# Performance work log

Measured on AMD Instinct MI355X. Metric: run time of the kernel, lower is better.

## Reference

```python
import jax, jax.numpy as jnp
import numpy as np

NW = 11       # num_windows per side
HEADS = 4
TOPK = 4
KVP = 4       # kv_per_window (adaptive maxpool output side)
BN_EPS = 1e-5
CLAMP = 0.12


def silu(x):
    return x * jax.nn.sigmoid(x)


def conv2d(x, w, b=None, groups=1, pad=0):
    y = jax.lax.conv_general_dilated(
        x, w, (1, 1), [(pad, pad), (pad, pad)],
        dimension_numbers=('NCHW', 'OIHW', 'NCHW'), feature_group_count=groups)
    if b is not None:
        y = y + b[None, :, None, None]
    return y


def grid_sample_bilinear(img, grid):
    # img (N,C,H,W), grid (N,Hg,Wg,2) in (x,y) order, align_corners=True.
    N, C, H, W = img.shape
    gx = (grid[..., 0] + 1.0) * 0.5 * (W - 1)
    gy = (grid[..., 1] + 1.0) * 0.5 * (H - 1)
    x0f = jnp.floor(gx)
    y0f = jnp.floor(gy)
    wx = (gx - x0f)[:, None]   # (N,1,Hg,Wg)
    wy = (gy - y0f)[:, None]
    x0 = jnp.clip(x0f.astype(jnp.int32), 0, W - 1)
    x1 = jnp.clip(x0 + 1, 0, W - 1)
    y0 = jnp.clip(y0f.astype(jnp.int32), 0, H - 1)
    y1 = jnp.clip(y0 + 1, 0, H - 1)
    gather = jax.vmap(lambda im, yi, xi: im[:, yi, xi])  # (C,Hg,Wg) per batch
    v00 = gather(img, y0, x0)
    v01 = gather(img, y0, x1)
    v10 = gather(img, y1, x0)
    v11 = gather(img, y1, x1)
    return (v00 * (1 - wx) * (1 - wy) + v01 * wx * (1 - wy)
            + v10 * (1 - wx) * wy + v11 * wx * wy)


def reference(x, q_w, q_b, kv_w, kv_b, off_dw_w, off_dw_b, off_bn_g, off_bn_b,
              off_pw_w, sec_w, sec_b):
    N, C, Hin, Win = x.shape
    pad_b = (-Hin) % NW
    pad_r = (-Win) % NW
    xp = jnp.pad(x, ((0, 0), (0, 0), (0, pad_b), (0, pad_r)))
    H, W = xp.shape[2], xp.shape[3]
    hw, ww = H // NW, W // NW
    p2, w2 = NW * NW, hw * ww
    qk_dim = C
    dh = C // HEADS
    scale = qk_dim ** (-0.5)

    # query projection (Conv+folded-BN+SiLU)
    q = silu(conv2d(xp, q_w, q_b))                       # (N,C,H,W)

    # deformable offset predictor: dwconv k9 -> BN(eval) -> 1x1 -> 2 channels
    t = conv2d(q, off_dw_w, off_dw_b, groups=C, pad=off_dw_w.shape[-1] // 2)
    t = (t / jnp.sqrt(1.0 + BN_EPS)) * off_bn_g[None, :, None, None] \
        + off_bn_b[None, :, None, None]
    offset = conv2d(t, off_pw_w)                         # (N,2,H,W)
    offset = jnp.transpose(offset, (0, 2, 3, 1))         # (N,H,W,2) as (y,x)

    # normalized reference points (torch linspace(0.5, s-0.5, s)/(s-1)*2-1)
    ry = jnp.linspace(0.5, H - 0.5, H) / (H - 1.0) * 2.0 - 1.0
    rx = jnp.linspace(0.5, W - 0.5, W) / (W - 1.0) * 2.0 - 1.0
    ref = jnp.stack(jnp.meshgrid(ry, rx, indexing='ij'), -1)  # (H,W,2) y,x
    pos = jnp.clip(offset + ref[None], -CLAMP, CLAMP)
    x_samp = grid_sample_bilinear(xp, pos[..., ::-1])    # grid in (x,y)

    kv = silu(conv2d(x_samp, kv_w, kv_b))                # (N,2C,H,W)

    def windowize(t):  # (N,Cc,H,W) -> (N,p2,hw,ww,Cc), p2 = j*NW+i
        Cc = t.shape[1]
        t = t.reshape(N, Cc, NW, hw, NW, ww)
        return jnp.transpose(t, (0, 2, 4, 3, 5, 1)).reshape(N, p2, hw, ww, Cc)

    q_win = windowize(q)                                 # (N,p2,hw,ww,C)
    kv_win = windowize(kv)                               # (N,p2,hw,ww,2C)

    # adaptive max-pool (hw,ww)->(KVP,KVP): evenly divisible here
    kvd = kv_win.reshape(N, p2, KVP, hw // KVP, KVP, ww // KVP, 2 * C)
    kvd = kvd.max(axis=(3, 5)).reshape(N, p2, KVP * KVP, 2 * C)

    # window-level top-k routing on detached window means
    qwin = jax.lax.stop_gradient(q_win.mean((2, 3)))                 # (N,p2,C)
    kwin = jax.lax.stop_gradient(kv_win[..., :qk_dim].mean((2, 3)))  # (N,p2,C)
    logit = jnp.einsum('npc,nqc->npq', qwin * scale, kwin)
    top_val, top_idx = jax.lax.top_k(logit, TOPK)        # (N,p2,TOPK)
    r_weight = jax.nn.softmax(top_val, -1)               # computed but unused (hard routing)

    # KV gather of routed windows
    kv_sel = kvd[jnp.arange(N)[:, None, None], top_idx]  # (N,p2,TOPK,16,2C)
    kw2 = TOPK * KVP * KVP
    k_sel = kv_sel[..., :qk_dim].reshape(N, p2, kw2, HEADS, dh)
    v_sel = kv_sel[..., qk_dim:].reshape(N, p2, kw2, HEADS, dh)
    q_pix = q_win.reshape(N, p2, w2, HEADS, dh)

    attn = jnp.einsum('npwhd,npkhd->nphwk', q_pix * scale, k_sel)
    attn = jax.nn.softmax(attn, -1)
    out = jnp.einsum('nphwk,npkhd->npwhd', attn, v_sel).reshape(N, p2, w2, C)

    # side conv enhancement on V, in full spatial layout
    v_full = kv_win[..., qk_dim:].reshape(N, NW, NW, hw, ww, C)
    v_full = jnp.transpose(v_full, (0, 5, 1, 3, 2, 4)).reshape(N, C, H, W)
    sec = conv2d(v_full, sec_w, sec_b, groups=C, pad=sec_w.shape[-1] // 2)
    sec = jnp.transpose(sec, (0, 2, 3, 1))               # (N,H,W,C)

    out = out.reshape(N, NW, NW, hw, ww, C)
    out = jnp.transpose(out, (0, 1, 3, 2, 4, 5)).reshape(N, H, W, C)
    out = (out + sec)[:, :Hin, :Win]
    return jnp.transpose(out, (0, 3, 1, 2))


def setup_inputs() -> dict:
    key = jax.random.key(0)
    ks = jax.random.split(key, 8)
    C = 128
    x = jax.random.normal(ks[0], (2, C, 352, 352), jnp.float32)
    q_w = jax.random.normal(ks[1], (C, C, 1, 1), jnp.float32) * 0.02
    q_b = jnp.zeros((C,), jnp.float32)
    kv_w = jax.random.normal(ks[2], (2 * C, C, 1, 1), jnp.float32) * 0.02
    kv_b = jnp.zeros((2 * C,), jnp.float32)
    off_dw_w = jax.random.normal(ks[3], (C, 1, 9, 9), jnp.float32) * 0.02
    off_dw_b = jnp.zeros((C,), jnp.float32)
    off_bn_g = jnp.ones((C,), jnp.float32)
    off_bn_b = jnp.zeros((C,), jnp.float32)
    off_pw_w = jax.random.normal(ks[4], (2, C, 1, 1), jnp.float32) * 0.02
    sec_w = jax.random.normal(ks[5], (C, 1, 3, 3), jnp.float32) * 0.02
    sec_b = jnp.zeros((C,), jnp.float32)
    return {'x': x, 'q_w': q_w, 'q_b': q_b, 'kv_w': kv_w, 'kv_b': kv_b,
            'off_dw_w': off_dw_w, 'off_dw_b': off_dw_b, 'off_bn_g': off_bn_g,
            'off_bn_b': off_bn_b, 'off_pw_w': off_pw_w, 'sec_w': sec_w,
            'sec_b': sec_b}
```

## Files before the change

### kernel.cpp

```cpp
#include <hip/hip_runtime.h>

#define HH 352
#define WWID 352
#define HW 123904
#define NIMG 2
#define C128 128
#define SCALE_F 0.08838834764831845f

typedef _Float16 f16x8 __attribute__((ext_vector_type(8)));
typedef float f32x4 __attribute__((ext_vector_type(4)));

__device__ __forceinline__ float silu_f(float v){ return v / (1.0f + __expf(-v)); }

__global__ __launch_bounds__(256) void k_wprep(const float* __restrict__ W,
                                               _Float16* __restrict__ Wf, int nct){
  int e = blockIdx.x*256 + threadIdx.x;
  if (e >= nct*256) return;
  int l = e & 63, kc = (e>>6)&3, ct = e>>8;
  const float* src = W + (size_t)(ct*16 + (l&15))*128 + kc*32 + (l>>4)*8;
  f16x8 pk;
#pragma unroll
  for (int j=0;j<8;j++) pk[j] = (_Float16)src[j];
  *(f16x8*)(Wf + (size_t)e*8) = pk;
}

template<int COW, bool SAMP, bool FUSEW, bool FUSEP>
__global__ __launch_bounds__(256) void k_conv_mfma(const float* __restrict__ X,
                                                   const float* __restrict__ samp,
                                                   const _Float16* __restrict__ Wf,
                                                   const float* __restrict__ B,
                                                   float* __restrict__ O,
                                                   float* __restrict__ winsum,
                                                   float* __restrict__ kvd2){
  constexpr int Cout = COW*4;
  constexpr int MT = COW/16;
  __shared__ _Float16 Xs[16*64*8];
  __shared__ int ibs[64];
  __shared__ float4 wls[64];
  const int t = threadIdx.x;
  const int bx = blockIdx.x;
  const int ty4 = (bx/22)*4, tx16 = (bx - (bx/22)*22)*16;
  const int n = blockIdx.z;
  const int wv = t>>6, l = t&63;
  const float* Xn = X + (size_t)n*C128*HW;
  if (SAMP){
    if (t < 64){
      int fr = ty4 + (t>>4), fc = tx16 + (t&15);
      size_t si = ((size_t)n*HW + (size_t)fr*WWID + fc)*2;
      float gx = samp[si + 0];
      float gy = samp[si + 1];
      float x0f = floorf(gx), y0f = floorf(gy);
      int x0 = (int)x0f, y0 = (int)y0f;
      float fx = gx - x0f, fy = gy - y0f;
      ibs[t] = y0*WWID + x0;
      wls[t] = make_float4((1.f-fx)*(1.f-fy), fx*(1.f-fy), (1.f-fx)*fy, fx*fy);
    }
    __syncthreads();
  }
  const int flatL = (ty4 + (l>>4))*WWID + tx16 + (l&15);
  int ib = 0; float4 wl = make_float4(0.f,0.f,0.f,0.f);
  if (SAMP){ ib = ibs[l]; wl = wls[l]; }
#pragma unroll
  for (int it=0; it<4; it++){
    int kb = it*4 + wv;
    f16x8 pk;
#pragma unroll
    for (int j=0;j<8;j++){
      int ci = kb*8 + j;
      float v;
      if (SAMP){
        const float* Xc = Xn + (size_t)ci*HW + ib;
        v = wl.x*Xc[0] + wl.y*Xc[1] + wl.z*Xc[WWID] + wl.w*Xc[WWID+1];
      } else {
        v = Xn[(size_t)ci*HW + flatL];
      }
      pk[j] = (_Float16)v;
    }
    *(f16x8*)(&Xs[(kb*64 + l)*8]) = pk;
  }
  __syncthreads();
  const int quad = l>>4, li = l&15;
  f32x4 acc[MT][4];
#pragma unroll
  for (int m=0;m<MT;m++)
#pragma unroll
    for (int nt=0;nt<4;nt++){ acc[m][nt][0]=0.f; acc[m][nt][1]=0.f; acc[m][nt][2]=0.f; acc[m][nt][3]=0.f; }
  const _Float16* Wfw = Wf + (size_t)(wv*MT)*4*64*8;
#pragma unroll
  for (int kc=0; kc<4; kc++){
    f16x8 b[4];
#pragma unroll
    for (int nt=0; nt<4; nt++)
      b[nt] = *(const f16x8*)(&Xs[((kc*4 + quad)*64 + nt*16 + li)*8]);
    f16x8 a[MT];
#pragma unroll
    for (int m=0;m<MT;m++)
      a[m] = *(const f16x8*)(Wfw + (size_t)((m*4 + kc)*64 + l)*8);
#pragma unroll
    for (int m=0;m<MT;m++)
#pragma unroll
      for (int nt=0;nt<4;nt++)
        acc[m][nt] = __builtin_amdgcn_mfma_f32_16x16x32_f16(a[m], b[nt], acc[m][nt], 0, 0, 0);
  }
  const int p = (ty4>>5)*11 + (tx16>>5);
#pragma unroll
  for (int m=0;m<MT;m++){
    int cob = wv*COW + m*16 + quad*4;
#pragma unroll
    for (int r=0;r<4;r++){
      int co = cob + r;
      float bb = B[co];
      float* Op = O + ((size_t)n*Cout + co)*HW + (size_t)ty4*WWID + tx16 + li;
      float ys[4];
#pragma unroll
      for (int nt=0;nt<4;nt++){
        float y = silu_f(acc[m][nt][r] + bb);
        ys[nt] = y;
        Op[nt*WWID] = y;
      }
      if (FUSEW && co < 128){
        float ssum = ys[0] + ys[1] + ys[2] + ys[3];
        ssum += __shfl_xor(ssum,1); ssum += __shfl_xor(ssum,2);
        ssum += __shfl_xor(ssum,4); ssum += __shfl_xor(ssum,8);
        if (li == 0)
          atomicAdd(winsum + ((size_t)n*121 + p)*128 + co, ssum);
      }
      if (FUSEP){
        float mx = fmaxf(fmaxf(ys[0],ys[1]), fmaxf(ys[2],ys[3]));
        mx = fmaxf(mx, __shfl_xor(mx,1));
        mx = fmaxf(mx, __shfl_xor(mx,2));
        mx = fmaxf(mx, __shfl_xor(mx,4));
        if ((li & 7) == 0){
          int cell = ((ty4>>3)&3)*4 + ((tx16>>3)&3) + (li>>3);
          int vh = (ty4>>2)&1;
          kvd2[((((size_t)n*121 + p)*16 + cell)*2 + vh)*256 + co] = mx;
        }
      }
    }
  }
}

__global__ __launch_bounds__(256) void k_offset_part(const float* __restrict__ q,
                                                     const float* __restrict__ dww,
                                                     const float* __restrict__ dwb,
                                                     const float* __restrict__ bng,
                                                     const float* __restrict__ bnb,
                                                     const float* __restrict__ pw,
                                                     float* __restrict__ offpart){
  __shared__ float s[4224];
  const int t = threadIdx.x;
  int id = blockIdx.x + 11*(blockIdx.y + 22*blockIdx.z);
  int lid = (id & 7)*242 + (id >> 3);
  int bx = lid % 11; int rest = lid / 11;
  int by = rest % 22; int zz = rest / 22;
  const int X0 = bx*32, Y0 = by*16;
  const int n = zz >> 2, cg = zz & 3, c0 = cg*32;
  const int w = __builtin_amdgcn_readfirstlane(t >> 6);
  const int l = t & 63;
  const int cg2 = l & 3, rowi = l >> 2;
  const float inv = 1.0f / sqrtf(1.0f + 1e-5f);
  const float* qn = q + (size_t)n*C128*HW;
  float o0[8], o1[8];
#pragma unroll
  for (int j=0;j<8;j++){ o0[j]=0.f; o1[j]=0.f; }
  float K0 = 0.f, K1 = 0.f;
  float pf[17];
  auto issue = [&](int stage){
    int cbase = c0 + stage*4;
#pragma unroll
    for (int i=0;i<17;i++){
      if (i == 16 && t >= 128) continue;
      int e = t + i*256;
      int ch = e/1056, idx = e - ch*1056;
      int rr = idx/44, cc = idx - rr*44;
      int gr = Y0 - 4 + rr, gc = X0 - 4 + cc;
      float v = 0.f;
      if (cc < 40 && gr>=0 && gr<HH && gc>=0 && gc<WWID)
        v = qn[(size_t)(cbase+ch)*HW + gr*WWID + gc];
      pf[i] = v;
    }
  };
  issue(0);
  for (int stage=0; stage<8; stage++){
    __syncthreads();
#pragma unroll
    for (int i=0;i<17;i++){
      if (i == 16 && t >= 128) continue;
      s[t + i*256] = pf[i];
    }
    __syncthreads();
    if (stage < 7) issue(stage+1);
    const int c = c0 + stage*4 + w;
    const float* wc = dww + c*81;
    const float* scp = s + w*1056 + rowi*44 + cg2*8;
    float sum[8];
#pragma unroll
    for (int j=0;j<8;j++) sum[j]=0.f;
#pragma unroll
    for (int r=0;r<9;r++){
      float f[16];
      const float4* s4 = (const float4*)(scp + r*44);
#pragma unroll
      for (int m2=0;m2<4;m2++){
        float4 v4 = s4[m2];
        f[4*m2]=v4.x; f[4*m2+1]=v4.y; f[4*m2+2]=v4.z; f[4*m2+3]=v4.w;
      }
#pragma unroll
      for (int k=0;k<9;k++){
        float wv = wc[r*9+k];
#pragma unroll
        for (int j=0;j<8;j++) sum[j] += wv * f[j+k];
      }
    }
    float g = inv*bng[c], bet = bnb[c], db = dwb[c];
    float p0c = pw[c], p1c = pw[C128+c];
    float A0 = p0c*g, A1 = p1c*g;
    float Cc = g*db + bet;
    K0 += p0c*Cc; K1 += p1c*Cc;
#pragma unroll
    for (int j=0;j<8;j++){ o0[j] += A0*sum[j]; o1[j] += A1*sum[j]; }
  }
  __syncthreads();
#pragma unroll
  for (int j=0;j<8;j++){
    s[w*1024 + l*16 + j]     = o0[j];
    s[w*1024 + l*16 + 8 + j] = o1[j];
  }
  if (l == 0){ s[4096 + w*2 + 0] = K0; s[4096 + w*2 + 1] = K1; }
  __syncthreads();
  float KT0 = s[4096+0]+s[4096+2]+s[4096+4]+s[4096+6];
  float KT1 = s[4096+1]+s[4096+3]+s[4096+5]+s[4096+7];
#pragma unroll
  for (int it2=0; it2<4; it2++){
    int e = t + it2*256;
    int slot = e >> 4, comp = e & 15;
    int scg2 = slot & 3, srow = slot >> 2;
    int out = comp >> 3, j = comp & 7;
    float v = s[0*1024 + slot*16 + comp] + s[1*1024 + slot*16 + comp]
            + s[2*1024 + slot*16 + comp] + s[3*1024 + slot*16 + comp];
    v += (out ? KT1 : KT0);
    int px = X0 + scg2*8 + j, py = Y0 + srow;
    offpart[(((size_t)cg*NIMG + n)*HW + (size_t)py*WWID + px)*2 + out] = v;
  }
}

__global__ __launch_bounds__(256) void k_samp_fin(const float* __restrict__ offpart,
                                                  float* __restrict__ samp){
  int e = blockIdx.x*256 + threadIdx.x;
  int n = e / HW, p = e - n*HW;
  int py = p / WWID, px = p - py*WWID;
  float oy = 0.f, ox = 0.f;
#pragma unroll
  for (int g=0; g<4; g++){
    float2 v = *(const float2*)(offpart + (((size_t)g*NIMG + n)*HW + p)*2);
    oy += v.x; ox += v.y;
  }
  const float k2 = 2.0f/351.0f;
  float ry = (0.5f+(float)py)*k2 - 1.0f, rx = (0.5f+(float)px)*k2 - 1.0f;
  float pyc = fminf(fmaxf(oy+ry,-0.12f),0.12f);
  float pxc = fminf(fmaxf(ox+rx,-0.12f),0.12f);
  float2 o; o.x = (pxc+1.f)*0.5f*351.f; o.y = (pyc+1.f)*0.5f*351.f;
  *(float2*)(samp + (size_t)e*2) = o;
}

__global__ __launch_bounds__(64) void k_routing(const float* __restrict__ qwin,
                                               const float* __restrict__ kwin,
                                               int* __restrict__ topidx){
  __shared__ float lg[128];
  const int p = blockIdx.x, n = blockIdx.y, l = threadIdx.x;
  const float* qr = qwin + ((size_t)n*121 + p)*128;
  const float* kb = kwin + (size_t)n*121*128;
  float a0 = 0.f, a1 = 0.f;
  const bool has1 = (l + 64) < 121;
  for (int c=0;c<128;c++){
    float qv = qr[c];
    a0 += qv * kb[(size_t)l*128 + c];
    if (has1) a1 += qv * kb[(size_t)(l+64)*128 + c];
  }
  lg[l] = a0;
  lg[64+l] = has1 ? a1 : -3.0e38f;
  __syncthreads();
  if (l == 0){
    for (int j=0;j<4;j++){
      float best = -3.0e38f; int bi = 0;
      for (int i=0;i<121;i++){ if (lg[i] > best){ best = lg[i]; bi = i; } }
      lg[bi] = -3.0e38f;
      topidx[((size_t)n*121 + p)*4 + j] = bi;
    }
  }
}

__global__ __launch_bounds__(256) void k_attention(const float* __restrict__ q,
                                                   const float* __restrict__ kvd2,
                                                   const int* __restrict__ topidx,
                                                   float* __restrict__ out){
  __shared__ float ks[64*32];
  __shared__ float vs[64*32];
  __shared__ int tix[4];
  const int p = blockIdx.x, n = blockIdx.y, h = blockIdx.z;
  const int t = threadIdx.x;
  if (t < 4) tix[t] = topidx[((size_t)n*121 + p)*4 + t];
  __syncthreads();
#pragma unroll
  for (int i=0;i<8;i++){
    int e = t + i*256;
    int d = e & 31, k = e >> 5;
    const float* kr = kvd2 + ((((size_t)(n*121) + tix[k>>4])*16 + (k & 15))*2)*256;
    ks[k*32 + d] = fmaxf(kr[h*32 + d],       kr[256 + h*32 + d]);
    vs[k*32 + d] = fmaxf(kr[128 + h*32 + d], kr[384 + h*32 + d]);
  }
  __syncthreads();
  const int py0 = (p/11)*32, px0 = (p%11)*32;
  const int wv = t >> 6, l = t & 63;
  const float* qh = q + ((size_t)n*C128 + h*32)*HW;
  float* oh = out + ((size_t)n*C128 + h*32)*HW;
  for (int it=0; it<2; it++){
    int pxa = it*512 + wv*128 + l;
    int pxb = pxa + 64;
    size_t offa = (size_t)(py0 + (pxa>>5))*WWID + px0 + (pxa&31);
    size_t offb = (size_t)(py0 + (pxb>>5))*WWID + px0 + (pxb&31);
    float qa[32], qb[32], oa[32], ob[32];
#pragma unroll
    for (int d=0; d<32; d++){
      qa[d] = qh[(size_t)d*HW + offa] * SCALE_F;
      qb[d] = qh[(size_t)d*HW + offb] * SCALE_F;
      oa[d] = 0.f; ob[d] = 0.f;
    }
    float suma = 0.f, sumb = 0.f;
    for (int k=0; k<64; k++){
      const float4* kk4 = (const float4*)(ks + k*32);
      float da = 0.f, db = 0.f;
#pragma unroll
      for (int d4=0; d4<8; d4++){
        float4 kk = kk4[d4];
        da += qa[d4*4+0]*kk.x + qa[d4*4+1]*kk.y + qa[d4*4+2]*kk.z + qa[d4*4+3]*kk.w;
        db += qb[d4*4+0]*kk.x + qb[d4*4+1]*kk.y + qb[d4*4+2]*kk.z + qb[d4*4+3]*kk.w;
      }
      float pa = __expf(da), pb = __expf(db);
      suma += pa; sumb += pb;
      const float4* vv4 = (const float4*)(vs + k*32);
#pragma unroll
      for (int d4=0; d4<8; d4++){
        float4 vvv = vv4[d4];
        oa[d4*4+0] += pa*vvv.x; oa[d4*4+1] += pa*vvv.y; oa[d4*4+2] += pa*vvv.z; oa[d4*4+3] += pa*vvv.w;
        ob[d4*4+0] += pb*vvv.x; ob[d4*4+1] += pb*vvv.y; ob[d4*4+2] += pb*vvv.z; ob[d4*4+3] += pb*vvv.w;
      }
    }
    float ia = 1.0f/suma, ib2 = 1.0f/sumb;
#pragma unroll
    for (int d=0; d<32; d++){
      oh[(size_t)d*HW + offa] = oa[d]*ia;
      oh[(size_t)d*HW + offb] = ob[d]*ib2;
    }
  }
}

__global__ __launch_bounds__(256) void k_sec_add(const float* __restrict__ kv,
                                                 const float* __restrict__ secw,
                                                 const float* __restrict__ secb,
                                                 float* __restrict__ out){
  __shared__ float s[34*34];
  const int t = threadIdx.x;
  const int bx = blockIdx.x, c = blockIdx.y, n = blockIdx.z;
  const int X0 = (bx % 11)*32, Y0 = (bx / 11)*32;
  const float* src = kv + ((size_t)n*256 + 128 + c)*HW;
  for (int e = t; e < 1156; e += 256){
    int row = e / 34;
    int col = e - row*34;
    int gr = Y0 - 1 + row, gc = X0 - 1 + col;
    s[e] = (gr >= 0 && gr < HH && gc >= 0 && gc < WWID) ? src[gr*WWID + gc] : 0.f;
  }
  __syncthreads();
  const int tx = (t & 7)*4, ty = t >> 3;
  float w[9];
#pragma unroll
  for (int i=0;i<9;i++) w[i] = secw[c*9 + i];
  float4 r = make_float4(0.f,0.f,0.f,0.f);
#pragma unroll
  for (int kr=0; kr<3; kr++){
    const float* row = s + (ty + kr)*34 + tx;
    float a0=row[0],a1=row[1],a2=row[2],a3=row[3],a4=row[4],a5=row[5];
    float w0=w[kr*3], w1=w[kr*3+1], w2=w[kr*3+2];
    r.x += w0*a0 + w1*a1 + w2*a2;
    r.y += w0*a1 + w1*a2 + w2*a3;
    r.z += w0*a2 + w1*a3 + w2*a4;
    r.w += w0*a3 + w1*a4 + w2*a5;
  }
  float bb = secb[c];
  float* op = out + ((size_t)n*C128 + c)*HW + (size_t)(Y0+ty)*WWID + X0 + tx;
  float4 cur = *(float4*)op;
  cur.x += r.x + bb; cur.y += r.y + bb; cur.z += r.z + bb; cur.w += r.w + bb;
  *(float4*)op = cur;
}

extern "C" void kernel_launch(void* const* d_in, const int* in_sizes, int n_in,
                              void* d_out, int out_size, void* d_ws, size_t ws_size,
                              hipStream_t stream) {
  const float* x        = (const float*)d_in[0];
  const float* q_w      = (const float*)d_in[1];
  const float* q_b      = (const float*)d_in[2];
  const float* kv_w     = (const float*)d_in[3];
  const float* kv_b     = (const float*)d_in[4];
  const float* off_dw_w = (const float*)d_in[5];
  const float* off_dw_b = (const float*)d_in[6];
  const float* off_bn_g = (const float*)d_in[7];
  const float* off_bn_b = (const float*)d_in[8];
  const float* off_pw_w = (const float*)d_in[9];
  const float* sec_w    = (const float*)d_in[10];
  const float* sec_b    = (const float*)d_in[11];
  float* outp = (float*)d_out;

  float* qbuf  = (float*)d_ws;
  float* kvbuf = qbuf  + (size_t)NIMG*C128*HW;
  float* samp  = kvbuf + (size_t)NIMG*256*HW;
  float* qwin  = samp  + (size_t)NIMG*HW*2;
  float* kwin  = qwin  + (size_t)NIMG*121*128;
  float* kvd2  = kwin  + (size_t)NIMG*121*128;
  int*   tidx  = (int*)(kvd2 + (size_t)NIMG*121*16*2*256);
  _Float16* wfq  = (_Float16*)(tidx + NIMG*121*4);
  _Float16* wfkv = wfq + 16384;
  float* offpart = kvbuf;

  hipMemsetAsync(qwin, 0, (size_t)NIMG*121*128*2*4, stream);

  k_wprep<<<dim3(8), 256, 0, stream>>>(q_w, wfq, 8);
  k_wprep<<<dim3(16), 256, 0, stream>>>(kv_w, wfkv, 16);
  k_conv_mfma<32, false, true, false><<<dim3(88*22, 1, NIMG), 256, 0, stream>>>(
      x, nullptr, wfq, q_b, qbuf, qwin, nullptr);
  k_offset_part<<<dim3(11, 22, NIMG*4), 256, 0, stream>>>(
      qbuf, off_dw_w, off_dw_b, off_bn_g, off_bn_b, off_pw_w, offpart);
  k_samp_fin<<<dim3(NIMG*HW/256), 256, 0, stream>>>(offpart, samp);
  k_conv_mfma<64, true, true, true><<<dim3(88*22, 1, NIMG), 256, 0, stream>>>(
      x, samp, wfkv, kv_b, kvbuf, kwin, kvd2);
  k_routing<<<dim3(121, NIMG), 64, 0, stream>>>(qwin, kwin, tidx);
  k_attention<<<dim3(121, NIMG, 4), 256, 0, stream>>>(qbuf, kvd2, tidx, outp);
  k_sec_add<<<dim3(121, 128, NIMG), 256, 0, stream>>>(kvbuf, sec_w, sec_b, outp);
}
```

Measured before the change: 823.5 us.

## Rewrite window attention with fp16 MFMA and split queries across more blocks

The attention kernel now stores K and a transposed V in shared memory as fp16. It computes QK^T and PV with 16x16x32 MFMA instructions, replacing the scalar fp32 dot-product loops, and moves probabilities between the two matmuls through a per-wave LDS buffer. The grid grows fourfold so each block handles a quarter of a window's queries, which adds parallelism but repeats the K/V gather per block. Softmax now subtracts the row max for stability, and fp16 inputs cost some precision.

```diff
diff --git a/kernel.cpp b/kernel.cpp
--- a/kernel.cpp
+++ b/kernel.cpp
@@ -8,6 +8,7 @@
 #define SCALE_F 0.08838834764831845f
 
 typedef _Float16 f16x8 __attribute__((ext_vector_type(8)));
+typedef _Float16 f16x4 __attribute__((ext_vector_type(4)));
 typedef float f32x4 __attribute__((ext_vector_type(4)));
 
 __device__ __forceinline__ float silu_f(float v){ return v / (1.0f + __expf(-v)); }
@@ -294,10 +295,12 @@
                                                    const float* __restrict__ kvd2,
                                                    const int* __restrict__ topidx,
                                                    float* __restrict__ out){
-  __shared__ float ks[64*32];
-  __shared__ float vs[64*32];
+  __shared__ _Float16 Ks[64*40];
+  __shared__ _Float16 Vs[32*72];
+  __shared__ _Float16 Ps[4*16*72];
   __shared__ int tix[4];
-  const int p = blockIdx.x, n = blockIdx.y, h = blockIdx.z;
+  const int p = blockIdx.x, n = blockIdx.y;
+  const int h = blockIdx.z & 3, qt = blockIdx.z >> 2;
   const int t = threadIdx.x;
   if (t < 4) tix[t] = topidx[((size_t)n*121 + p)*4 + t];
   __syncthreads();
@@ -306,51 +309,69 @@
     int e = t + i*256;
     int d = e & 31, k = e >> 5;
     const float* kr = kvd2 + ((((size_t)(n*121) + tix[k>>4])*16 + (k & 15))*2)*256;
-    ks[k*32 + d] = fmaxf(kr[h*32 + d],       kr[256 + h*32 + d]);
-    vs[k*32 + d] = fmaxf(kr[128 + h*32 + d], kr[384 + h*32 + d]);
+    float kk = fmaxf(kr[h*32 + d],       kr[256 + h*32 + d]);
+    float vv = fmaxf(kr[128 + h*32 + d], kr[384 + h*32 + d]);
+    Ks[k*40 + d] = (_Float16)kk;
+    Vs[d*72 + k] = (_Float16)vv;
   }
   __syncthreads();
   const int py0 = (p/11)*32, px0 = (p%11)*32;
-  const int wv = t >> 6, l = t & 63;
+  const int w = t >> 6, l = t & 63;
+  const int li = l & 15, qd = l >> 4;
   const float* qh = q + ((size_t)n*C128 + h*32)*HW;
   float* oh = out + ((size_t)n*C128 + h*32)*HW;
-  for (int it=0; it<2; it++){
-    int pxa = it*512 + wv*128 + l;
-    int pxb = pxa + 64;
-    size_t offa = (size_t)(py0 + (pxa>>5))*WWID + px0 + (pxa&31);
-    size_t offb = (size_t)(py0 + (pxb>>5))*WWID + px0 + (pxb&31);
-    float qa[32], qb[32], oa[32], ob[32];
-#pragma unroll
-    for (int d=0; d<32; d++){
-      qa[d] = qh[(size_t)d*HW + offa] * SCALE_F;
-      qb[d] = qh[(size_t)d*HW + offb] * SCALE_F;
-      oa[d] = 0.f; ob[d] = 0.f;
-    }
-    float suma = 0.f, sumb = 0.f;
-    for (int k=0; k<64; k++){
-      const float4* kk4 = (const float4*)(ks + k*32);
-      float da = 0.f, db = 0.f;
-#pragma unroll
-      for (int d4=0; d4<8; d4++){
-        float4 kk = kk4[d4];
-        da += qa[d4*4+0]*kk.x + qa[d4*4+1]*kk.y + qa[d4*4+2]*kk.z + qa[d4*4+3]*kk.w;
-        db += qb[d4*4+0]*kk.x + qb[d4*4+1]*kk.y + qb[d4*4+2]*kk.z + qb[d4*4+3]*kk.w;
-      }
-      float pa = __expf(da), pb = __expf(db);
-      suma += pa; sumb += pb;
-      const float4* vv4 = (const float4*)(vs + k*32);
-#pragma unroll
-      for (int d4=0; d4<8; d4++){
-        float4 vvv = vv4[d4];
-        oa[d4*4+0] += pa*vvv.x; oa[d4*4+1] += pa*vvv.y; oa[d4*4+2] += pa*vvv.z; oa[d4*4+3] += pa*vvv.w;
-        ob[d4*4+0] += pb*vvv.x; ob[d4*4+1] += pb*vvv.y; ob[d4*4+2] += pb*vvv.z; ob[d4*4+3] += pb*vvv.w;
-      }
-    }
-    float ia = 1.0f/suma, ib2 = 1.0f/sumb;
-#pragma unroll
-    for (int d=0; d<32; d++){
-      oh[(size_t)d*HW + offa] = oa[d]*ia;
-      oh[(size_t)d*HW + offb] = ob[d]*ib2;
+  _Float16* Pw = Ps + w*16*72;
+  for (int it=0; it<4; it++){
+    int g = qt*16 + it*4 + w;
+    size_t base = (size_t)(py0 + (g>>1))*WWID + px0 + (g&1)*16 + li;
+    f16x8 qa;
+#pragma unroll
+    for (int j=0;j<8;j++)
+      qa[j] = (_Float16)(qh[(size_t)(qd*8+j)*HW + base] * SCALE_F);
+    f32x4 S[4];
+#pragma unroll
+    for (int nt=0;nt<4;nt++){
+      f16x8 ka = *(const f16x8*)(Ks + (nt*16 + li)*40 + qd*8);
+      f32x4 z; z[0]=0.f; z[1]=0.f; z[2]=0.f; z[3]=0.f;
+      S[nt] = __builtin_amdgcn_mfma_f32_16x16x32_f16(ka, qa, z, 0, 0, 0);
+    }
+    float m = -3.0e38f;
+#pragma unroll
+    for (int nt=0;nt<4;nt++)
+#pragma unroll
+      for (int r=0;r<4;r++) m = fmaxf(m, S[nt][r]);
+    m = fmaxf(m, __shfl_xor(m, 16));
+    m = fmaxf(m, __shfl_xor(m, 32));
+    float sum = 0.f;
+#pragma unroll
+    for (int nt=0;nt<4;nt++){
+      f16x4 pk;
+#pragma unroll
+      for (int r=0;r<4;r++){
+        float e = __expf(S[nt][r] - m);
+        sum += e;
+        pk[r] = (_Float16)e;
+      }
+      *(f16x4*)(Pw + li*72 + nt*16 + qd*4) = pk;
+    }
+    sum += __shfl_xor(sum, 16);
+    sum += __shfl_xor(sum, 32);
+    float inv = 1.0f / sum;
+    f32x4 a0, a1;
+    a0[0]=0.f;a0[1]=0.f;a0[2]=0.f;a0[3]=0.f;
+    a1[0]=0.f;a1[1]=0.f;a1[2]=0.f;a1[3]=0.f;
+#pragma unroll
+    for (int c=0;c<2;c++){
+      f16x8 pb  = *(const f16x8*)(Pw + li*72        + c*32 + qd*8);
+      f16x8 va0 = *(const f16x8*)(Vs + li*72        + c*32 + qd*8);
+      f16x8 va1 = *(const f16x8*)(Vs + (16+li)*72   + c*32 + qd*8);
+      a0 = __builtin_amdgcn_mfma_f32_16x16x32_f16(va0, pb, a0, 0, 0, 0);
+      a1 = __builtin_amdgcn_mfma_f32_16x16x32_f16(va1, pb, a1, 0, 0, 0);
+    }
+#pragma unroll
+    for (int r=0;r<4;r++){
+      oh[(size_t)(qd*4+r)*HW + base]        = a0[r]*inv;
+      oh[(size_t)(16+qd*4+r)*HW + base]     = a1[r]*inv;
     }
   }
 }
@@ -433,6 +454,6 @@
   k_conv_mfma<64, true, true, true><<<dim3(88*22, 1, NIMG), 256, 0, stream>>>(
       x, samp, wfkv, kv_b, kvbuf, kwin, kvd2);
   k_routing<<<dim3(121, NIMG), 64, 0, stream>>>(qwin, kwin, tidx);
-  k_attention<<<dim3(121, NIMG, 4), 256, 0, stream>>>(qbuf, kvd2, tidx, outp);
+  k_attention<<<dim3(121, NIMG, 16), 256, 0, stream>>>(qbuf, kvd2, tidx, outp);
   k_sec_add<<<dim3(121, 128, NIMG), 256, 0, stream>>>(kvbuf, sec_w, sec_b, outp);
 }
```

Measured after the change: 726.7 us. 1.13x faster.
